# Kernel optimization log

Hardware: AMD Instinct MI355X
Metric: run time of the kernel (lower is better)

The kernel has to match this reference:

```python
import jax, jax.numpy as jnp
import numpy as np

N = 50000      # nodes
E = 800000     # edges
D = 128        # node feature dim
H = 128        # hid_channel (hardcoded in module)
B = 64         # graphs in batch
C = 3          # num_classes (COLLAB)
K = N // 2     # TopKPooling ratio=0.5


def setup_inputs() -> dict:
    key = jax.random.key(0)
    ks = jax.random.split(key, 16)
    s = 0.05
    return {
        "x": jax.random.normal(ks[0], (N, D), dtype=jnp.float32),
        "edge_index": jax.random.randint(ks[1], (E, 2), 0, N),
        "batch": jnp.sort(jax.random.randint(ks[2], (N,), 0, B)),
        "W1": jax.random.normal(ks[3], (D, H), dtype=jnp.float32) * s,
        "b1": jnp.zeros((H,), jnp.float32),
        "W2": jax.random.normal(ks[4], (H, H), dtype=jnp.float32) * s,
        "b2": jnp.zeros((H,), jnp.float32),
        "p": jax.random.normal(ks[5], (H,), dtype=jnp.float32),
        "W3": jax.random.normal(ks[6], (H, H), dtype=jnp.float32) * s,
        "b3": jnp.zeros((H,), jnp.float32),
        "W4": jax.random.normal(ks[7], (H, H), dtype=jnp.float32) * s,
        "b4": jnp.zeros((H,), jnp.float32),
        "fcW1": jax.random.normal(ks[8], (H, H), dtype=jnp.float32) * s,
        "fcb1": jnp.zeros((H,), jnp.float32),
        "fcW2": jax.random.normal(ks[9], (H, C), dtype=jnp.float32) * s,
        "fcb2": jnp.zeros((C,), jnp.float32),
    }


def gcn_conv(x, src, dst, ew, W, b, n):
    # PyG GCNConv: D^{-1/2}(A+I)D^{-1/2} x W + b, deg includes self-loop
    h = x @ W
    deg = jax.ops.segment_sum(ew, dst, num_segments=n) + 1.0
    dinv = jax.lax.rsqrt(deg)
    coef = dinv[src] * dinv[dst] * ew            # [E]
    agg = jax.ops.segment_sum(coef[:, None] * h[src], dst, num_segments=n)
    return agg + (dinv * dinv)[:, None] * h + b  # self-loop term + bias


def reference(x, edge_index, batch, W1, b1, W2, b2, p, W3, b3, W4, b4, fcW1, fcb1, fcW2, fcb2):
    src, dst = edge_index[:, 0], edge_index[:, 1]
    ew = jnp.ones((E,), x.dtype)

    h = jax.nn.relu(gcn_conv(x, src, dst, ew, W1, b1, N))
    h = jax.nn.relu(gcn_conv(h, src, dst, ew, W2, b2, N))

    # TopKPooling: score = x.p/||p||, keep top K, gate by tanh(score)
    score = h @ p / jnp.linalg.norm(p)
    top_vals, perm = jax.lax.top_k(score, K)
    hp = h[perm] * jnp.tanh(top_vals)[:, None]
    batch_p = batch[perm]
    new_idx = jnp.full((N,), -1, jnp.int32).at[perm].set(jnp.arange(K, dtype=jnp.int32))
    ns, nd = new_idx[src], new_idx[dst]
    mask = (ns >= 0) & (nd >= 0)
    ewp = mask.astype(x.dtype)
    ns = jnp.where(mask, ns, 0)
    nd = jnp.where(mask, nd, 0)

    h = jax.nn.relu(gcn_conv(hp, ns, nd, ewp, W3, b3, K))
    h = jax.nn.relu(gcn_conv(h, ns, nd, ewp, W4, b4, K))

    # global mean pool over graphs
    sums = jax.ops.segment_sum(h, batch_p, num_segments=B)
    cnt = jax.ops.segment_sum(jnp.ones((K,), x.dtype), batch_p, num_segments=B)
    g = sums / jnp.maximum(cnt, 1.0)[:, None]

    g = jax.nn.relu(g @ fcW1 + fcb1)
    logits = g @ fcW2 + fcb2
    return jax.nn.log_softmax(logits, axis=1)
```

## Files before the change

### kernel.cpp

```cpp
#include <hip/hip_runtime.h>

#define N_NODES 50000
#define N_EDGES 800000
#define HDIM    128
#define NBATCH  64
#define NCLS    3
#define KSEL    (N_NODES/2)
#define MMB_ROWS 64
#define HIST_BLOCKS 128
#define POOL_BLOCKS 256
#define POOL_CHUNK  ((KSEL + POOL_BLOCKS - 1) / POOL_BLOCKS)
#define NBUCK ((N_NODES + 127) >> 7)
#define EPB   2048
#define S1_BLOCKS ((N_EDGES + EPB - 1) / EPB)
#define SEG_CAP 4096

typedef unsigned long long u64;
typedef unsigned int u32;
typedef unsigned short ushort_t;
typedef _Float16 half8 __attribute__((ext_vector_type(8)));
typedef float floatx4 __attribute__((ext_vector_type(4)));

struct SelState { u64 prefix; int krem; int cnt; };

__device__ __forceinline__ float h2f(ushort_t u) {
    _Float16 h = *(_Float16*)&u;
    return (float)h;
}

__global__ void init_pnorm_k(const float* __restrict__ p, float* __restrict__ pn,
        SelState* st) {
    __shared__ float red[HDIM];
    int t = threadIdx.x;
    float v = p[t];
    red[t] = v * v;
    __syncthreads();
    for (int s = HDIM/2; s > 0; s >>= 1) {
        if (t < s) red[t] += red[t+s];
        __syncthreads();
    }
    pn[t] = v / sqrtf(red[0]);
    if (t == 0) { st->prefix = 0ull; st->krem = KSEL; st->cnt = 0; }
}

__global__ void deg_full_k(const int* __restrict__ ei, int* __restrict__ degi) {
    int e = blockIdx.x * blockDim.x + threadIdx.x;
    if (e >= N_EDGES) return;
    int2 ed = ((const int2*)ei)[e];
    atomicAdd(&degi[ed.y], 1);
}

__global__ __launch_bounds__(256) void scan12_k(const int* __restrict__ degi,
        int* __restrict__ bsum, int* __restrict__ boff, float* __restrict__ dinv,
        int* __restrict__ rowptr, int n, int nb, int* done) {
    __shared__ int sh[256];
    __shared__ int lastf;
    int t = threadIdx.x;
    int i = blockIdx.x * 256 + t;
    int d = (i < n) ? degi[i] : 0;
    if (i < n) dinv[i] = rsqrtf((float)d + 1.0f);
    sh[t] = d;
    __syncthreads();
    for (int s = 128; s > 0; s >>= 1) {
        if (t < s) sh[t] += sh[t + s];
        __syncthreads();
    }
    if (t == 0) {
        atomicExch(&bsum[blockIdx.x], sh[0]);
        __threadfence();
        int dd = atomicAdd(done, 1);
        lastf = (dd == (int)gridDim.x - 1) ? 1 : 0;
    }
    __syncthreads();
    if (lastf) {
        int v = (t < nb) ? atomicAdd(&bsum[t], 0) : 0;
        sh[t] = v;
        __syncthreads();
        for (int dl = 1; dl < 256; dl <<= 1) {
            int u = (t >= dl) ? sh[t - dl] : 0;
            __syncthreads();
            sh[t] += u;
            __syncthreads();
        }
        if (t < nb) boff[t] = sh[t] - v;
        if (t == 255) rowptr[n] = sh[255];
    }
}

__global__ __launch_bounds__(256) void scan3_k(const int* __restrict__ degi,
        const int* __restrict__ boff, int* __restrict__ rowptr, int n) {
    __shared__ int sh[256];
    int t = threadIdx.x;
    int i = blockIdx.x * 256 + t;
    int v = (i < n) ? degi[i] : 0;
    sh[t] = v;
    __syncthreads();
    for (int d = 1; d < 256; d <<= 1) {
        int u = (t >= d) ? sh[t - d] : 0;
        __syncthreads();
        sh[t] += u;
        __syncthreads();
    }
    if (i < n) rowptr[i] = boff[blockIdx.x] + sh[t] - v;
}

__global__ __launch_bounds__(256) void csr_bucket_k(const int* __restrict__ ei,
        const int* __restrict__ rowptr, u32* __restrict__ gcnt, u32* __restrict__ ebuf) {
    __shared__ u32 bh[NBUCK];
    __shared__ u32 cursor[NBUCK];
    int t = threadIdx.x;
    for (int i = t; i < NBUCK; i += 256) bh[i] = 0;
    __syncthreads();
    int e0 = blockIdx.x * EPB;
    int2 ed[8]; int nb[8];
#pragma unroll
    for (int i = 0; i < 8; ++i) {
        int e = e0 + t + i * 256;
        if (e < N_EDGES) {
            ed[i] = ((const int2*)ei)[e];
            nb[i] = ed[i].y >> 7;
            atomicAdd(&bh[nb[i]], 1u);
        } else nb[i] = -1;
    }
    __syncthreads();
    for (int b = t; b < NBUCK; b += 256) {
        u32 c = bh[b];
        if (c) cursor[b] = (u32)rowptr[b << 7] + atomicAdd(&gcnt[b], c);
    }
    __syncthreads();
#pragma unroll
    for (int i = 0; i < 8; ++i) {
        if (nb[i] >= 0) {
            u32 pos = atomicAdd(&cursor[nb[i]], 1u);
            ebuf[pos] = ((u32)(ed[i].y & 127) << 16) | (u32)ed[i].x;
        }
    }
}

__global__ __launch_bounds__(256) void csr_build_k(const u32* __restrict__ ebuf,
        const int* __restrict__ rowptr, int* __restrict__ csr) {
    __shared__ int rp[129];
    __shared__ int fcnt[128];
    __shared__ int seg[SEG_CAP];
    int b = blockIdx.x;
    int lo = b << 7;
    int nn = min(128, N_NODES - lo);
    int t = threadIdx.x;
    if (t <= nn) rp[t] = rowptr[lo + t];
    if (t < 128) fcnt[t] = 0;
    __syncthreads();
    int segbase = rp[0];
    int segsz = rp[nn] - segbase;
    if (segsz <= SEG_CAP) {
        for (int idx = t; idx < segsz; idx += 256) {
            u32 v = ebuf[segbase + idx];
            int dl = v >> 16;
            int slot = rp[dl] - segbase + atomicAdd(&fcnt[dl], 1);
            seg[slot] = (int)(v & 0xFFFFu);
        }
        __syncthreads();
        for (int idx = t; idx < segsz; idx += 256) csr[segbase + idx] = seg[idx];
    } else {
        for (int idx = t; idx < segsz; idx += 256) {
            u32 v = ebuf[segbase + idx];
            int dl = v >> 16;
            int slot = rp[dl] + atomicAdd(&fcnt[dl], 1);
            csr[slot] = (int)(v & 0xFFFFu);
        }
    }
}

__global__ __launch_bounds__(256) void gather_k(const int* __restrict__ rowptr,
        const int* __restrict__ csr, const float* __restrict__ dinv,
        const ushort_t* __restrict__ hb, const float* __restrict__ bias,
        float* __restrict__ out, int n) {
    int node = blockIdx.x * 4 + (threadIdx.x >> 6);
    if (node >= n) return;
    int lane = threadIdx.x & 63;
    float di = dinv[node];
    float2 bv = *(const float2*)&bias[2*lane];
    ushort2 hs = *(const ushort2*)&hb[(size_t)node * HDIM + 2*lane];
    float s2 = di * di;
    float accx = s2 * h2f(hs.x) + bv.x;
    float accy = s2 * h2f(hs.y) + bv.y;
    int rs = rowptr[node], re = rowptr[node + 1];
    for (int base = rs; base < re; base += 64) {
        int cnt = min(64, re - base);
        int srcv = 0; float cv = 0.0f;
        if (lane < cnt) { srcv = csr[base + lane]; cv = di * dinv[srcv]; }
        int j = 0;
        for (; j + 8 <= cnt; j += 8) {
            int s0 = __shfl(srcv, j+0, 64); int s1 = __shfl(srcv, j+1, 64);
            int s2i= __shfl(srcv, j+2, 64); int s3 = __shfl(srcv, j+3, 64);
            int s4 = __shfl(srcv, j+4, 64); int s5 = __shfl(srcv, j+5, 64);
            int s6 = __shfl(srcv, j+6, 64); int s7 = __shfl(srcv, j+7, 64);
            float c0 = __shfl(cv, j+0, 64); float c1 = __shfl(cv, j+1, 64);
            float c2 = __shfl(cv, j+2, 64); float c3 = __shfl(cv, j+3, 64);
            float c4 = __shfl(cv, j+4, 64); float c5 = __shfl(cv, j+5, 64);
            float c6 = __shfl(cv, j+6, 64); float c7 = __shfl(cv, j+7, 64);
            ushort2 v0 = *(const ushort2*)&hb[(size_t)s0 * HDIM + 2*lane];
            ushort2 v1 = *(const ushort2*)&hb[(size_t)s1 * HDIM + 2*lane];
            ushort2 v2 = *(const ushort2*)&hb[(size_t)s2i* HDIM + 2*lane];
            ushort2 v3 = *(const ushort2*)&hb[(size_t)s3 * HDIM + 2*lane];
            ushort2 v4 = *(const ushort2*)&hb[(size_t)s4 * HDIM + 2*lane];
            ushort2 v5 = *(const ushort2*)&hb[(size_t)s5 * HDIM + 2*lane];
            ushort2 v6 = *(const ushort2*)&hb[(size_t)s6 * HDIM + 2*lane];
            ushort2 v7 = *(const ushort2*)&hb[(size_t)s7 * HDIM + 2*lane];
            accx += c0*h2f(v0.x); accy += c0*h2f(v0.y);
            accx += c1*h2f(v1.x); accy += c1*h2f(v1.y);
            accx += c2*h2f(v2.x); accy += c2*h2f(v2.y);
            accx += c3*h2f(v3.x); accy += c3*h2f(v3.y);
            accx += c4*h2f(v4.x); accy += c4*h2f(v4.y);
            accx += c5*h2f(v5.x); accy += c5*h2f(v5.y);
            accx += c6*h2f(v6.x); accy += c6*h2f(v6.y);
            accx += c7*h2f(v7.x); accy += c7*h2f(v7.y);
        }
        for (; j < cnt; ++j) {
            int src = __shfl(srcv, j, 64);
            float c  = __shfl(cv, j, 64);
            ushort2 sv = *(const ushort2*)&hb[(size_t)src * HDIM + 2*lane];
            accx += c * h2f(sv.x);
            accy += c * h2f(sv.y);
        }
    }
    float2 o; o.x = accx; o.y = accy;
    *(float2*)&out[(size_t)node * HDIM + 2*lane] = o;
}

__global__ __launch_bounds__(256) void gather_pool_k(const int* __restrict__ rowptr,
        const int* __restrict__ csr, const int* __restrict__ n2o,
        const int2* __restrict__ pinfo, const float* __restrict__ dinvp,
        const ushort_t* __restrict__ hb, const float* __restrict__ bias,
        float* __restrict__ out) {
    __shared__ int   sns[4][64];
    __shared__ float scf[4][64];
    int k = blockIdx.x * 4 + (threadIdx.x >> 6);
    if (k >= KSEL) return;
    int wid = threadIdx.x >> 6, lane = threadIdx.x & 63;
    float di = dinvp[k];
    float2 bv = *(const float2*)&bias[2*lane];
    ushort2 hs = *(const ushort2*)&hb[(size_t)k * HDIM + 2*lane];
    float s2 = di * di;
    float accx = s2 * h2f(hs.x) + bv.x;
    float accy = s2 * h2f(hs.y) + bv.y;
    int old = n2o[k];
    int rs = rowptr[old], re = rowptr[old + 1];
    for (int base = rs; base < re; base += 64) {
        int span = min(64, re - base);
        int ns = -1; float dv = 0.0f;
        if (lane < span) {
            int2 pi = pinfo[csr[base + lane]];
            ns = pi.x; dv = __int_as_float(pi.y);
        }
        bool sel = (ns >= 0);
        u64 m = __ballot(sel);
        int rank = __popcll(m & ((1ull << lane) - 1ull));
        if (sel) { sns[wid][rank] = ns; scf[wid][rank] = di * dv; }
        int cnt = __popcll(m);
        __threadfence_block();
        int j = 0;
        for (; j + 8 <= cnt; j += 8) {
            int s0 = sns[wid][j+0]; int s1 = sns[wid][j+1];
            int s2i= sns[wid][j+2]; int s3 = sns[wid][j+3];
            int s4 = sns[wid][j+4]; int s5 = sns[wid][j+5];
            int s6 = sns[wid][j+6]; int s7 = sns[wid][j+7];
            float c0 = scf[wid][j+0]; float c1 = scf[wid][j+1];
            float c2 = scf[wid][j+2]; float c3 = scf[wid][j+3];
            float c4 = scf[wid][j+4]; float c5 = scf[wid][j+5];
            float c6 = scf[wid][j+6]; float c7 = scf[wid][j+7];
            ushort2 v0 = *(const ushort2*)&hb[(size_t)s0 * HDIM + 2*lane];
            ushort2 v1 = *(const ushort2*)&hb[(size_t)s1 * HDIM + 2*lane];
            ushort2 v2 = *(const ushort2*)&hb[(size_t)s2i* HDIM + 2*lane];
            ushort2 v3 = *(const ushort2*)&hb[(size_t)s3 * HDIM + 2*lane];
            ushort2 v4 = *(const ushort2*)&hb[(size_t)s4 * HDIM + 2*lane];
            ushort2 v5 = *(const ushort2*)&hb[(size_t)s5 * HDIM + 2*lane];
            ushort2 v6 = *(const ushort2*)&hb[(size_t)s6 * HDIM + 2*lane];
            ushort2 v7 = *(const ushort2*)&hb[(size_t)s7 * HDIM + 2*lane];
            accx += c0*h2f(v0.x); accy += c0*h2f(v0.y);
            accx += c1*h2f(v1.x); accy += c1*h2f(v1.y);
            accx += c2*h2f(v2.x); accy += c2*h2f(v2.y);
            accx += c3*h2f(v3.x); accy += c3*h2f(v3.y);
            accx += c4*h2f(v4.x); accy += c4*h2f(v4.y);
            accx += c5*h2f(v5.x); accy += c5*h2f(v5.y);
            accx += c6*h2f(v6.x); accy += c6*h2f(v6.y);
            accx += c7*h2f(v7.x); accy += c7*h2f(v7.y);
        }
        for (; j < cnt; ++j) {
            int src = sns[wid][j];
            float c = scf[wid][j];
            ushort2 sv = *(const ushort2*)&hb[(size_t)src * HDIM + 2*lane];
            accx += c * h2f(sv.x);
            accy += c * h2f(sv.y);
        }
    }
    float2 o; o.x = accx; o.y = accy;
    *(float2*)&out[(size_t)k * HDIM + 2*lane] = o;
}

template<bool RELU_IN>
__global__ __launch_bounds__(256) void matmul_k(const float* __restrict__ in,
        const float* __restrict__ W, ushort_t* __restrict__ outb, int rows) {
    __shared__ _Float16 Wf[4][8][64][8];
    int t = threadIdx.x;
    int rbase = blockIdx.x * MMB_ROWS;
    for (int idx = t; idx < HDIM * HDIM; idx += 256) {
        int k = idx >> 7, j = idx & 127;
        int kk = k >> 5, kgrp = (k >> 3) & 3, i = k & 7;
        int ct = j >> 4, lrow = j & 15;
        Wf[kk][ct][kgrp * 16 + lrow][i] = (_Float16)W[idx];
    }
    int wid = t >> 6, lane = t & 63;
    int lrow = lane & 15, kgrp = lane >> 4;
    int arow = rbase + wid * 16 + lrow;
    bool rowok = (arow < rows);
    const float* arp = in + (size_t)(rowok ? arow : 0) * HDIM + kgrp * 8;
    half8 a[4];
#pragma unroll
    for (int kk = 0; kk < 4; ++kk) {
        float4 lo = rowok ? *(const float4*)(arp + kk * 32)     : float4{0,0,0,0};
        float4 hi = rowok ? *(const float4*)(arp + kk * 32 + 4) : float4{0,0,0,0};
        if (RELU_IN) {
            lo.x = fmaxf(lo.x, 0.f); lo.y = fmaxf(lo.y, 0.f);
            lo.z = fmaxf(lo.z, 0.f); lo.w = fmaxf(lo.w, 0.f);
            hi.x = fmaxf(hi.x, 0.f); hi.y = fmaxf(hi.y, 0.f);
            hi.z = fmaxf(hi.z, 0.f); hi.w = fmaxf(hi.w, 0.f);
        }
        a[kk][0] = (_Float16)lo.x; a[kk][1] = (_Float16)lo.y;
        a[kk][2] = (_Float16)lo.z; a[kk][3] = (_Float16)lo.w;
        a[kk][4] = (_Float16)hi.x; a[kk][5] = (_Float16)hi.y;
        a[kk][6] = (_Float16)hi.z; a[kk][7] = (_Float16)hi.w;
    }
    __syncthreads();
    floatx4 zero4 = {0.0f, 0.0f, 0.0f, 0.0f};
    floatx4 acc[8];
#pragma unroll
    for (int ct = 0; ct < 8; ++ct) acc[ct] = zero4;
#pragma unroll
    for (int kk = 0; kk < 4; ++kk) {
#pragma unroll
        for (int ct = 0; ct < 8; ++ct) {
            half8 b = *(const half8*)&Wf[kk][ct][lane][0];
            acc[ct] = __builtin_amdgcn_mfma_f32_16x16x32_f16(a[kk], b, acc[ct], 0, 0, 0);
        }
    }
    int orow0 = rbase + wid * 16 + kgrp * 4;
#pragma unroll
    for (int ct = 0; ct < 8; ++ct) {
#pragma unroll
        for (int i = 0; i < 4; ++i) {
            int row = orow0 + i;
            if (row < rows) {
                _Float16 hv = (_Float16)acc[ct][i];
                outb[(size_t)row * HDIM + ct * 16 + lrow] = *(ushort_t*)&hv;
            }
        }
    }
}

__global__ void score_key_k(const float* __restrict__ h, const float* __restrict__ pn,
        float* __restrict__ score, u64* __restrict__ key) {
    int gid  = blockIdx.x * blockDim.x + threadIdx.x;
    int node = gid >> 6;
    int lane = gid & 63;
    if (node >= N_NODES) return;
    const float* row = h + (size_t)node * HDIM;
    float sv = fmaxf(row[lane], 0.f) * pn[lane] + fmaxf(row[lane+64], 0.f) * pn[lane+64];
#pragma unroll
    for (int o = 32; o > 0; o >>= 1) sv += __shfl_xor(sv, o, 64);
    if (lane == 0) {
        score[node] = sv;
        u32 u = __float_as_uint(sv);
        u = (u & 0x80000000u) ? ~u : (u | 0x80000000u);
        key[node] = ((u64)u << 16) | (u64)(65535 - node);
    }
}

__global__ __launch_bounds__(256) void histscan_k(const u64* __restrict__ key,
        SelState* st, u32* __restrict__ hist, int pass, int* done) {
    __shared__ u32 lh[256];
    __shared__ int lastf;
    int t = threadIdx.x;
    lh[t] = 0;
    __syncthreads();
    int dsh = 40 - 8 * pass;
    u64 pref = st->prefix;
    for (int i = blockIdx.x * 256 + t; i < N_NODES; i += HIST_BLOCKS * 256) {
        u64 k = key[i];
        if (((k ^ pref) >> (dsh + 8)) == 0)
            atomicAdd(&lh[(int)((k >> dsh) & 255)], 1u);
    }
    __syncthreads();
    u32 v = lh[t];
    if (v) atomicAdd(&hist[pass * 256 + t], v);
    __threadfence();
    __syncthreads();
    if (t == 0) {
        int dd = atomicAdd(done, 1);
        lastf = (dd == HIST_BLOCKS - 1) ? 1 : 0;
    }
    __syncthreads();
    if (lastf) {
        lh[t] = atomicAdd(&hist[pass * 256 + t], 0u);
        __syncthreads();
        if (t == 0) {
            int krem = st->krem;
            int b = 255;
            for (; b > 0; --b) {
                int cnt = (int)lh[b];
                if (cnt < krem) krem -= cnt;
                else break;
            }
            st->prefix |= ((u64)b) << dsh;
            st->krem = krem;
        }
    }
}

__global__ void select_k(const u64* __restrict__ key, SelState* st,
        int2* __restrict__ pinfo, int* __restrict__ n2o) {
    int i = blockIdx.x * blockDim.x + threadIdx.x;
    if (i >= N_NODES) return;
    if (key[i] >= st->prefix) {
        int pos = atomicAdd(&st->cnt, 1);
        pinfo[i].x = pos;
        n2o[pos] = i;
    } else {
        pinfo[i].x = -1;
    }
}

__global__ void hp_k(const float* __restrict__ h2, const float* __restrict__ score,
        const int* __restrict__ n2o, float* __restrict__ hp) {
    int gid = blockIdx.x * blockDim.x + threadIdx.x;
    if (gid >= KSEL * 32) return;
    int k  = gid >> 5;
    int c4 = (gid & 31) << 2;
    int old = n2o[k];
    float tv = tanhf(score[old]);
    float4 hv = *(const float4*)&h2[(size_t)old * HDIM + c4];
    float4 o;
    o.x = fmaxf(hv.x, 0.f) * tv;
    o.y = fmaxf(hv.y, 0.f) * tv;
    o.z = fmaxf(hv.z, 0.f) * tv;
    o.w = fmaxf(hv.w, 0.f) * tv;
    *(float4*)&hp[(size_t)k * HDIM + c4] = o;
}

__global__ __launch_bounds__(256) void pool_deg_k(const int* __restrict__ rowptr,
        const int* __restrict__ csr, const int* __restrict__ n2o,
        int2* __restrict__ pinfo, float* __restrict__ dinvp) {
    int k = blockIdx.x * 4 + (threadIdx.x >> 6);
    if (k >= KSEL) return;
    int lane = threadIdx.x & 63;
    int old = n2o[k];
    int rs = rowptr[old], re = rowptr[old + 1];
    int cnt = 0;
    for (int base = rs; base < re; base += 64) {
        int span = min(64, re - base);
        bool sel = false;
        if (lane < span) sel = (pinfo[csr[base + lane]].x >= 0);
        cnt += __popcll(__ballot(sel));
    }
    if (lane == 0) {
        float dv = rsqrtf((float)cnt + 1.0f);
        dinvp[k] = dv;
        pinfo[old].y = __float_as_int(dv);
    }
}

__global__ __launch_bounds__(256) void pool_stage1_k(const float* __restrict__ h,
        const int* __restrict__ n2o, const int* __restrict__ batch,
        float* __restrict__ partial, int* __restrict__ pcnt) {
    __shared__ float ls[NBATCH * HDIM];
    __shared__ int   lc[NBATCH];
    int t = threadIdx.x;
    for (int i = t; i < NBATCH * HDIM; i += 256) ls[i] = 0.0f;
    if (t < NBATCH) lc[t] = 0;
    __syncthreads();
    int wid = t >> 6, lane = t & 63;
    int start = blockIdx.x * POOL_CHUNK;
    int end = min(start + POOL_CHUNK, KSEL);
    for (int k = start + wid; k < end; k += 4) {
        int b = batch[n2o[k]];
        float2 hv = *(const float2*)&h[(size_t)k * HDIM + 2*lane];
        atomicAdd(&ls[b * HDIM + 2*lane],     fmaxf(hv.x, 0.0f));
        atomicAdd(&ls[b * HDIM + 2*lane + 1], fmaxf(hv.y, 0.0f));
        if (lane == 0) atomicAdd(&lc[b], 1);
    }
    __syncthreads();
    float* pb = partial + (size_t)blockIdx.x * (NBATCH * HDIM);
    for (int i = t; i < NBATCH * HDIM; i += 256) pb[i] = ls[i];
    if (t < NBATCH) pcnt[blockIdx.x * NBATCH + t] = lc[t];
}

__global__ __launch_bounds__(256) void pool_stage2_k(const float* __restrict__ partial,
        const int* __restrict__ pcnt, float* __restrict__ sums, float* __restrict__ cntb) {
    int i = blockIdx.x * 256 + threadIdx.x;
    if (i >= NBATCH * HDIM) return;
    float s = 0.0f;
    for (int p = 0; p < POOL_BLOCKS; ++p) s += partial[(size_t)p * NBATCH * HDIM + i];
    sums[i] = s;
    if (i < NBATCH) {
        int c = 0;
        for (int p = 0; p < POOL_BLOCKS; ++p) c += pcnt[p * NBATCH + i];
        cntb[i] = (float)c;
    }
}

__global__ __launch_bounds__(256) void fc_k(const float* __restrict__ sums,
        const float* __restrict__ cntb, const float* __restrict__ W1b,
        const float* __restrict__ b1b, const float* __restrict__ W2b,
        const float* __restrict__ b2b, float* __restrict__ gbuf,
        float* __restrict__ out, int* done) {
    int t = threadIdx.x;
    int gid = blockIdx.x * 256 + t;
    if (gid < NBATCH * HDIM) {
        int b = gid >> 7, j = gid & 127;
        float inv = 1.0f / fmaxf(cntb[b], 1.0f);
        float acc = 0.0f;
        for (int k = 0; k < HDIM; ++k) acc += sums[b * HDIM + k] * W1b[k * HDIM + j];
        gbuf[gid] = fmaxf(acc * inv + b1b[j], 0.0f);
    }
    __threadfence();
    __shared__ int lastf;
    if (t == 0) lastf = (atomicAdd(done, 1) == (int)gridDim.x - 1) ? 1 : 0;
    __syncthreads();
    if (!lastf || t >= NBATCH) return;
    __threadfence();
    int b = t;
    float l[NCLS];
    for (int c = 0; c < NCLS; ++c) {
        float acc = b2b[c];
        for (int k = 0; k < HDIM; ++k) acc += gbuf[b * HDIM + k] * W2b[k * NCLS + c];
        l[c] = acc;
    }
    float m = fmaxf(l[0], fmaxf(l[1], l[2]));
    float sum = expf(l[0]-m) + expf(l[1]-m) + expf(l[2]-m);
    float ls = logf(sum);
    for (int c = 0; c < NCLS; ++c) out[b * NCLS + c] = l[c] - m - ls;
}

extern "C" void kernel_launch(void* const* d_in, const int* in_sizes, int n_in,
                              void* d_out, int out_size, void* d_ws, size_t ws_size,
                              hipStream_t stream) {
    const float* x    = (const float*)d_in[0];
    const int*   ei   = (const int*)d_in[1];
    const int*   batch= (const int*)d_in[2];
    const float* W1   = (const float*)d_in[3];
    const float* b1   = (const float*)d_in[4];
    const float* W2   = (const float*)d_in[5];
    const float* b2   = (const float*)d_in[6];
    const float* p    = (const float*)d_in[7];
    const float* W3   = (const float*)d_in[8];
    const float* b3   = (const float*)d_in[9];
    const float* W4   = (const float*)d_in[10];
    const float* b4   = (const float*)d_in[11];
    const float* fcW1 = (const float*)d_in[12];
    const float* fcb1 = (const float*)d_in[13];
    const float* fcW2 = (const float*)d_in[14];
    const float* fcb2 = (const float*)d_in[15];
    float* out = (float*)d_out;

    char* ws = (char*)d_ws;
    size_t off = 0;
    auto alloc = [&](size_t bytes) {
        size_t r = off;
        off = (off + bytes + 255) & ~(size_t)255;
        return r;
    };
    float* A     = (float*)(ws + alloc((size_t)N_NODES * HDIM * 4));
    float* Bf    = (float*)(ws + alloc((size_t)N_NODES * HDIM * 4));
    ushort_t* Hbf= (ushort_t*)(ws + alloc((size_t)N_NODES * HDIM * 2));
    u64*   key   = (u64*)  (ws + alloc((size_t)N_NODES * 8));
    float* score = (float*)(ws + alloc((size_t)N_NODES * 4));
    int2*  pinfo = (int2*) (ws + alloc((size_t)N_NODES * 8));
    int*   n2o   = (int*)  (ws + alloc((size_t)KSEL * 4));
    float* pn    = (float*)(ws + alloc(HDIM * 4));
    float* gbuf  = (float*)(ws + alloc(NBATCH * HDIM * 4));
    SelState* st = (SelState*)(ws + alloc(256));
    float* dinv1 = (float*)(ws + alloc((size_t)N_NODES * 4));
    float* dinvp = (float*)(ws + alloc((size_t)KSEL * 4));
    int*   rowptr= (int*)  (ws + alloc((size_t)(N_NODES + 1) * 4));
    int*   csr   = (int*)  (ws + alloc((size_t)N_EDGES * 4));
    u32*   ebuf  = (u32*)  (ws + alloc((size_t)N_EDGES * 4));
    int*   bsum  = (int*)  (ws + alloc(256 * 4));
    int*   boff  = (int*)  (ws + alloc(256 * 4));
    float* partial=(float*)(ws + alloc((size_t)POOL_BLOCKS * NBATCH * HDIM * 4));
    int*   pcnt  = (int*)  (ws + alloc((size_t)POOL_BLOCKS * NBATCH * 4));
    float* sums  = (float*)(ws + alloc(NBATCH * HDIM * 4));
    float* cntb  = (float*)(ws + alloc(NBATCH * 4));
    size_t z1 = off;
    int*   degi  = (int*)(ws + alloc((size_t)N_NODES * 4));
    u32*   gcnt  = (u32*)(ws + alloc((size_t)NBUCK * 4));
    u32*   hist  = (u32*)(ws + alloc(6 * 256 * 4));
    int*   done  = (int*)(ws + alloc(16 * 4));
    size_t z1e = off;

    hipMemsetAsync(ws + z1, 0, z1e - z1, stream);
    init_pnorm_k<<<1, HDIM, 0, stream>>>(p, pn, st);

    const int eg   = (N_EDGES + 255) / 256;
    const int ng   = (N_NODES + 255) / 256;
    const int mm_grid_n = (N_NODES + MMB_ROWS - 1) / MMB_ROWS;
    const int mm_grid_k = (KSEL + MMB_ROWS - 1) / MMB_ROWS;
    const int gt_grid_n = (N_NODES + 3) / 4;
    const int gt_grid_k = (KSEL + 3) / 4;
    const int kh4_grid  = (KSEL * 32 + 255) / 256;

    deg_full_k<<<eg, 256, 0, stream>>>(ei, degi);
    scan12_k<<<ng, 256, 0, stream>>>(degi, bsum, boff, dinv1, rowptr, N_NODES, ng, done + 0);
    scan3_k<<<ng, 256, 0, stream>>>(degi, boff, rowptr, N_NODES);
    csr_bucket_k<<<S1_BLOCKS, 256, 0, stream>>>(ei, rowptr, gcnt, ebuf);
    csr_build_k<<<NBUCK, 256, 0, stream>>>(ebuf, rowptr, csr);

    matmul_k<false><<<mm_grid_n, 256, 0, stream>>>(x, W1, Hbf, N_NODES);
    gather_k<<<gt_grid_n, 256, 0, stream>>>(rowptr, csr, dinv1, Hbf, b1, Bf, N_NODES);
    matmul_k<true><<<mm_grid_n, 256, 0, stream>>>(Bf, W2, Hbf, N_NODES);
    gather_k<<<gt_grid_n, 256, 0, stream>>>(rowptr, csr, dinv1, Hbf, b2, Bf, N_NODES);

    score_key_k<<<(N_NODES * 64 + 255) / 256, 256, 0, stream>>>(Bf, pn, score, key);
    for (int pass = 0; pass < 6; ++pass)
        histscan_k<<<HIST_BLOCKS, 256, 0, stream>>>(key, st, hist, pass, done + 2 + pass);
    select_k<<<ng, 256, 0, stream>>>(key, st, pinfo, n2o);
    hp_k<<<kh4_grid, 256, 0, stream>>>(Bf, score, n2o, A);

    pool_deg_k<<<gt_grid_k, 256, 0, stream>>>(rowptr, csr, n2o, pinfo, dinvp);

    matmul_k<false><<<mm_grid_k, 256, 0, stream>>>(A, W3, Hbf, KSEL);
    gather_pool_k<<<gt_grid_k, 256, 0, stream>>>(rowptr, csr, n2o, pinfo, dinvp, Hbf, b3, Bf);
    matmul_k<true><<<mm_grid_k, 256, 0, stream>>>(Bf, W4, Hbf, KSEL);
    gather_pool_k<<<gt_grid_k, 256, 0, stream>>>(rowptr, csr, n2o, pinfo, dinvp, Hbf, b4, A);

    pool_stage1_k<<<POOL_BLOCKS, 256, 0, stream>>>(A, n2o, batch, partial, pcnt);
    pool_stage2_k<<<(NBATCH * HDIM + 255) / 256, 256, 0, stream>>>(partial, pcnt, sums, cntb);
    fc_k<<<(NBATCH * HDIM + 255) / 256, 256, 0, stream>>>(sums, cntb, fcW1, fcb1,
                                                          fcW2, fcb2, gbuf, out, done + 8);
}
```

Measured before the change: 424.1 us.

## Fuse scoring into gather, widen radix select to 12 bits, merge hp and pool-degree kernels

Computes the TopK score and sort key inside the second GCN gather kernel, so the separate score pass that re-read the feature matrix is no longer needed. The radix select now uses 4096-bin histograms over 4 passes instead of 256 bins over 6. Bin selection becomes a parallel block scan instead of a serial loop in one thread. The gating of pooled features is also fused into the pool-degree kernel, dropping another launch and one read of the selected rows. The cost is more shared-memory atomics and larger histograms to clear and flush in each select pass.

```diff
diff --git a/kernel.cpp b/kernel.cpp
--- a/kernel.cpp
+++ b/kernel.cpp
@@ -8,6 +8,7 @@
 #define KSEL    (N_NODES/2)
 #define MMB_ROWS 64
 #define HIST_BLOCKS 128
+#define RBINS 4096
 #define POOL_BLOCKS 256
 #define POOL_CHUNK  ((KSEL + POOL_BLOCKS - 1) / POOL_BLOCKS)
 #define NBUCK ((N_NODES + 127) >> 7)
@@ -170,10 +171,12 @@
     }
 }
 
+template<bool SCORE>
 __global__ __launch_bounds__(256) void gather_k(const int* __restrict__ rowptr,
         const int* __restrict__ csr, const float* __restrict__ dinv,
         const ushort_t* __restrict__ hb, const float* __restrict__ bias,
-        float* __restrict__ out, int n) {
+        float* __restrict__ out, int n, const float* __restrict__ pn,
+        float* __restrict__ score, u64* __restrict__ keyv) {
     int node = blockIdx.x * 4 + (threadIdx.x >> 6);
     if (node >= n) return;
     int lane = threadIdx.x & 63;
@@ -225,6 +228,18 @@
     }
     float2 o; o.x = accx; o.y = accy;
     *(float2*)&out[(size_t)node * HDIM + 2*lane] = o;
+    if (SCORE) {
+        float2 pv = *(const float2*)&pn[2*lane];
+        float sv = fmaxf(accx, 0.f) * pv.x + fmaxf(accy, 0.f) * pv.y;
+#pragma unroll
+        for (int os = 32; os > 0; os >>= 1) sv += __shfl_xor(sv, os, 64);
+        if (lane == 0) {
+            score[node] = sv;
+            u32 u = __float_as_uint(sv);
+            u = (u & 0x80000000u) ? ~u : (u | 0x80000000u);
+            keyv[node] = ((u64)u << 16) | (u64)(65535 - node);
+        }
+    }
 }
 
 __global__ __launch_bounds__(256) void gather_pool_k(const int* __restrict__ rowptr,
@@ -357,41 +372,26 @@
     }
 }
 
-__global__ void score_key_k(const float* __restrict__ h, const float* __restrict__ pn,
-        float* __restrict__ score, u64* __restrict__ key) {
-    int gid  = blockIdx.x * blockDim.x + threadIdx.x;
-    int node = gid >> 6;
-    int lane = gid & 63;
-    if (node >= N_NODES) return;
-    const float* row = h + (size_t)node * HDIM;
-    float sv = fmaxf(row[lane], 0.f) * pn[lane] + fmaxf(row[lane+64], 0.f) * pn[lane+64];
-#pragma unroll
-    for (int o = 32; o > 0; o >>= 1) sv += __shfl_xor(sv, o, 64);
-    if (lane == 0) {
-        score[node] = sv;
-        u32 u = __float_as_uint(sv);
-        u = (u & 0x80000000u) ? ~u : (u | 0x80000000u);
-        key[node] = ((u64)u << 16) | (u64)(65535 - node);
-    }
-}
-
 __global__ __launch_bounds__(256) void histscan_k(const u64* __restrict__ key,
         SelState* st, u32* __restrict__ hist, int pass, int* done) {
-    __shared__ u32 lh[256];
+    __shared__ u32 lh[RBINS];
+    __shared__ u32 sct[256];
     __shared__ int lastf;
     int t = threadIdx.x;
-    lh[t] = 0;
-    __syncthreads();
-    int dsh = 40 - 8 * pass;
+    for (int b = t; b < RBINS; b += 256) lh[b] = 0;
+    __syncthreads();
+    int dsh = 36 - 12 * pass;
     u64 pref = st->prefix;
     for (int i = blockIdx.x * 256 + t; i < N_NODES; i += HIST_BLOCKS * 256) {
         u64 k = key[i];
-        if (((k ^ pref) >> (dsh + 8)) == 0)
-            atomicAdd(&lh[(int)((k >> dsh) & 255)], 1u);
-    }
-    __syncthreads();
-    u32 v = lh[t];
-    if (v) atomicAdd(&hist[pass * 256 + t], v);
+        if (((k ^ pref) >> (dsh + 12)) == 0)
+            atomicAdd(&lh[(int)((k >> dsh) & 4095)], 1u);
+    }
+    __syncthreads();
+    for (int b = t; b < RBINS; b += 256) {
+        u32 v = lh[b];
+        if (v) atomicAdd(&hist[pass * RBINS + b], v);
+    }
     __threadfence();
     __syncthreads();
     if (t == 0) {
@@ -400,18 +400,34 @@
     }
     __syncthreads();
     if (lastf) {
-        lh[t] = atomicAdd(&hist[pass * 256 + t], 0u);
-        __syncthreads();
-        if (t == 0) {
-            int krem = st->krem;
-            int b = 255;
-            for (; b > 0; --b) {
-                int cnt = (int)lh[b];
-                if (cnt < krem) krem -= cnt;
-                else break;
+        for (int b = t; b < RBINS; b += 256)
+            lh[b] = atomicAdd(&hist[pass * RBINS + b], 0u);
+        __syncthreads();
+        int krem = st->krem;
+        u32 ctt = 0;
+#pragma unroll
+        for (int j = 0; j < 16; ++j) ctt += lh[t * 16 + j];
+        sct[t] = ctt;
+        __syncthreads();
+        for (int d = 1; d < 256; d <<= 1) {
+            u32 add = (t + d < 256) ? sct[t + d] : 0u;
+            __syncthreads();
+            sct[t] += add;
+            __syncthreads();
+        }
+        u32 incl = sct[t];
+        u32 excl = incl - ctt;
+        if ((int)excl < krem && (int)incl >= krem) {
+            u32 run = excl;
+            int bsel = 0; u32 csel = 0;
+            for (int j = 15; j >= 0; --j) {
+                u32 c = lh[t * 16 + j];
+                run += c;
+                if ((int)run >= krem) { bsel = t * 16 + j; csel = c; break; }
             }
-            st->prefix |= ((u64)b) << dsh;
-            st->krem = krem;
+            int newk = krem - (int)(run - csel);
+            st->prefix = pref | ((u64)bsel << dsh);
+            st->krem = newk;
         }
     }
 }
@@ -429,30 +445,18 @@
     }
 }
 
-__global__ void hp_k(const float* __restrict__ h2, const float* __restrict__ score,
-        const int* __restrict__ n2o, float* __restrict__ hp) {
-    int gid = blockIdx.x * blockDim.x + threadIdx.x;
-    if (gid >= KSEL * 32) return;
-    int k  = gid >> 5;
-    int c4 = (gid & 31) << 2;
-    int old = n2o[k];
-    float tv = tanhf(score[old]);
-    float4 hv = *(const float4*)&h2[(size_t)old * HDIM + c4];
-    float4 o;
-    o.x = fmaxf(hv.x, 0.f) * tv;
-    o.y = fmaxf(hv.y, 0.f) * tv;
-    o.z = fmaxf(hv.z, 0.f) * tv;
-    o.w = fmaxf(hv.w, 0.f) * tv;
-    *(float4*)&hp[(size_t)k * HDIM + c4] = o;
-}
-
-__global__ __launch_bounds__(256) void pool_deg_k(const int* __restrict__ rowptr,
-        const int* __restrict__ csr, const int* __restrict__ n2o,
-        int2* __restrict__ pinfo, float* __restrict__ dinvp) {
+__global__ __launch_bounds__(256) void hp_pool_k(const float* __restrict__ h2,
+        const float* __restrict__ score, const int* __restrict__ n2o,
+        const int* __restrict__ rowptr, const int* __restrict__ csr,
+        int2* __restrict__ pinfo, float* __restrict__ dinvp, float* __restrict__ hp) {
     int k = blockIdx.x * 4 + (threadIdx.x >> 6);
     if (k >= KSEL) return;
     int lane = threadIdx.x & 63;
     int old = n2o[k];
+    float tv = tanhf(score[old]);
+    const float* row = h2 + (size_t)old * HDIM;
+    hp[(size_t)k * HDIM + lane]      = fmaxf(row[lane], 0.f) * tv;
+    hp[(size_t)k * HDIM + lane + 64] = fmaxf(row[lane+64], 0.f) * tv;
     int rs = rowptr[old], re = rowptr[old + 1];
     int cnt = 0;
     for (int base = rs; base < re; base += 64) {
@@ -592,7 +596,7 @@
     size_t z1 = off;
     int*   degi  = (int*)(ws + alloc((size_t)N_NODES * 4));
     u32*   gcnt  = (u32*)(ws + alloc((size_t)NBUCK * 4));
-    u32*   hist  = (u32*)(ws + alloc(6 * 256 * 4));
+    u32*   hist  = (u32*)(ws + alloc(4 * RBINS * 4));
     int*   done  = (int*)(ws + alloc(16 * 4));
     size_t z1e = off;
 
@@ -605,7 +609,6 @@
     const int mm_grid_k = (KSEL + MMB_ROWS - 1) / MMB_ROWS;
     const int gt_grid_n = (N_NODES + 3) / 4;
     const int gt_grid_k = (KSEL + 3) / 4;
-    const int kh4_grid  = (KSEL * 32 + 255) / 256;
 
     deg_full_k<<<eg, 256, 0, stream>>>(ei, degi);
     scan12_k<<<ng, 256, 0, stream>>>(degi, bsum, boff, dinv1, rowptr, N_NODES, ng, done + 0);
@@ -614,17 +617,17 @@
     csr_build_k<<<NBUCK, 256, 0, stream>>>(ebuf, rowptr, csr);
 
     matmul_k<false><<<mm_grid_n, 256, 0, stream>>>(x, W1, Hbf, N_NODES);
-    gather_k<<<gt_grid_n, 256, 0, stream>>>(rowptr, csr, dinv1, Hbf, b1, Bf, N_NODES);
+    gather_k<false><<<gt_grid_n, 256, 0, stream>>>(rowptr, csr, dinv1, Hbf, b1, Bf,
+                                                   N_NODES, nullptr, nullptr, nullptr);
     matmul_k<true><<<mm_grid_n, 256, 0, stream>>>(Bf, W2, Hbf, N_NODES);
-    gather_k<<<gt_grid_n, 256, 0, stream>>>(rowptr, csr, dinv1, Hbf, b2, Bf, N_NODES);
-
-    score_key_k<<<(N_NODES * 64 + 255) / 256, 256, 0, stream>>>(Bf, pn, score, key);
-    for (int pass = 0; pass < 6; ++pass)
+    gather_k<true><<<gt_grid_n, 256, 0, stream>>>(rowptr, csr, dinv1, Hbf, b2, Bf,
+                                                  N_NODES, pn, score, key);
+
+    for (int pass = 0; pass < 4; ++pass)
         histscan_k<<<HIST_BLOCKS, 256, 0, stream>>>(key, st, hist, pass, done + 2 + pass);
     select_k<<<ng, 256, 0, stream>>>(key, st, pinfo, n2o);
-    hp_k<<<kh4_grid, 256, 0, stream>>>(Bf, score, n2o, A);
-
-    pool_deg_k<<<gt_grid_k, 256, 0, stream>>>(rowptr, csr, n2o, pinfo, dinvp);
+
+    hp_pool_k<<<gt_grid_k, 256, 0, stream>>>(Bf, score, n2o, rowptr, csr, pinfo, dinvp, A);
 
     matmul_k<false><<<mm_grid_k, 256, 0, stream>>>(A, W3, Hbf, KSEL);
     gather_pool_k<<<gt_grid_k, 256, 0, stream>>>(rowptr, csr, n2o, pinfo, dinvp, Hbf, b3, Bf);
```

Result: faster. 377.0 us (-11.1%).
